# Performance work log

Measured on AMD Instinct MI355X. Metric: run time of the kernel, lower is better.

## Reference

```python
import jax, jax.numpy as jnp
import numpy as np

N, E, F, H, G = 50000, 640000, 128, 128, 64


def setup_inputs() -> dict:
    key = jax.random.key(0)
    ks = jax.random.split(key, 10)
    x = jax.random.normal(ks[0], (N, F), dtype=jnp.float32)
    edge_index = jax.random.randint(ks[1], (2, E), 0, N)
    batch = jnp.sort(jax.random.randint(ks[2], (N,), 0, G))

    def glorot(k, shp):
        return jax.random.normal(k, shp, dtype=jnp.float32) * np.float32(1.0 / np.sqrt(shp[0]))

    W1 = glorot(ks[3], (F, H)); b1 = jnp.zeros((H,), jnp.float32)
    W2 = glorot(ks[4], (H, H)); b2 = jnp.zeros((H,), jnp.float32)
    W3 = glorot(ks[5], (H, H)); b3 = jnp.zeros((H,), jnp.float32)
    W4 = glorot(ks[6], (H, 2)); b4 = jnp.zeros((2,), jnp.float32)
    return {"x": x, "W1": W1, "b1": b1, "W2": W2, "b2": b2,
            "W3": W3, "b3": b3, "W4": W4, "b4": b4,
            "edge_index": edge_index, "batch": batch, "num_graphs": G}


def reference(x, W1, b1, W2, b2, W3, b3, W4, b4, edge_index, batch, num_graphs):
    n = x.shape[0]
    loop = jnp.arange(n, dtype=edge_index.dtype)
    src = jnp.concatenate([edge_index[0], loop])  # with self-loops (PyG GCNConv default)
    dst = jnp.concatenate([edge_index[1], loop])
    # symmetric degree normalization: D^{-1/2} (A+I) D^{-1/2}
    deg = jax.ops.segment_sum(jnp.ones_like(src, dtype=x.dtype), dst, num_segments=n)
    dinv = jnp.where(deg > 0, jax.lax.rsqrt(deg), 0.0)
    norm = (dinv[src] * dinv[dst])[:, None]  # [E+N, 1]

    def gcn_conv(h, W, b):
        m = h @ W                                   # transform first (F->H), then propagate
        agg = jax.ops.segment_sum(m[src] * norm, dst, num_segments=n)
        return agg + b

    h = jax.nn.relu(gcn_conv(x, W1, b1))
    h = jax.nn.relu(gcn_conv(h, W2, b2))
    g = jax.ops.segment_max(h, batch, num_segments=num_graphs)  # global_max_pool
    z = jax.nn.relu(g @ W3 + b3)                    # dropout is identity in eval
    logits = z @ W4 + b4
    return jax.nn.log_softmax(logits, axis=1)
```

## Files before the change

kernel.cpp:

```cpp
#include <hip/hip_runtime.h>
#include <hip/hip_bf16.h>
#include <math.h>

#define HDIM 128
#define SCAN_B 256
#define NBLK 256

typedef short bfrag __attribute__((ext_vector_type(8)));
typedef float f32x4 __attribute__((ext_vector_type(4)));

__device__ inline unsigned short f2bf_rne(float x) {
    unsigned u = __float_as_uint(x);
    u = (u + 0x7fffu + ((u >> 16) & 1u)) >> 16;
    return (unsigned short)u;
}
__device__ inline float bf_lo(unsigned u) { return __uint_as_float(u << 16); }
__device__ inline float bf_hi(unsigned u) { return __uint_as_float(u & 0xffff0000u); }
__device__ inline unsigned bf_pack(float lo, float hi) {
    return ((unsigned)f2bf_rne(hi) << 16) | (unsigned)f2bf_rne(lo);
}


__device__ inline void hist_body(int b, const int* __restrict__ dst,
                                 int* __restrict__ hist, int E, int chunk, int nbuck) {
    __shared__ int hl[256];
    int t = threadIdx.x;
    hl[t] = 0;
    __syncthreads();
    int start = b * chunk, end = min(E, start + chunk);
    for (int e = start + t; e < end; e += 256) atomicAdd(&hl[dst[e] >> 8], 1);
    __syncthreads();
    if (t < nbuck) hist[t * NBLK + b] = hl[t];
}

__device__ inline void wfrag_body(int b, const float* __restrict__ W1,
                                  const float* __restrict__ W2,
                                  unsigned short* __restrict__ w1h,
                                  unsigned short* __restrict__ w1l,
                                  unsigned short* __restrict__ w2h,
                                  unsigned short* __restrict__ w2l) {
    const float* W = (b < 64) ? W1 : W2;
    unsigned short* whi = (b < 64) ? w1h : w2h;
    unsigned short* wlo = (b < 64) ? w1l : w2l;
    int idx = (b & 63) * 256 + threadIdx.x;
    int k = idx >> 7;
    int n = idx & 127;
    int kt = k >> 5, q = (k >> 3) & 3, j = k & 7;
    int lm = n >> 3, nt = n & 7;
    int lane = q * 16 + lm;
    int o = ((kt * 8 + nt) * 64 + lane) * 8 + j;
    float x = W[idx];
    unsigned short hb = f2bf_rne(x);
    float hf = __uint_as_float(((unsigned)hb) << 16);
    unsigned short lb = f2bf_rne(x - hf);
    whi[o] = hb;
    wlo[o] = lb;
}

__device__ inline void scatter_body(int b, const int* __restrict__ srcv,
                                    const int* __restrict__ dstv,
                                    const int* __restrict__ hscan,
                                    int2* __restrict__ sorted,
                                    int E, int chunk, int nbuck) {
    __shared__ int cur[256];
    int t = threadIdx.x;
    if (t < nbuck) cur[t] = hscan[t * NBLK + b];
    __syncthreads();
    int start = b * chunk, end = min(E, start + chunk);
    for (int e = start + t; e < end; e += 256) {
        int d = dstv[e];
        int pos = atomicAdd(&cur[d >> 8], 1);
        sorted[pos] = make_int2(srcv[e], d);
    }
}

#define GBM 64
__device__ inline void gemm_f32_body(int b, const float* __restrict__ A,
                                     const unsigned short* __restrict__ whi,
                                     const unsigned short* __restrict__ wlo,
                                     unsigned short* __restrict__ C, int Nrows) {
    int tid = threadIdx.x;
    int w = tid >> 6, L = tid & 63;
    int lm = L & 15, lq = L >> 4;
    int row0 = b * GBM + w * 16;

    f32x4 acc[8];
#pragma unroll
    for (int nt = 0; nt < 8; ++nt) acc[nt] = (f32x4)(0.f);

#pragma unroll
    for (int kt = 0; kt < 4; ++kt) {
        int gr = row0 + lm;
        float4 v0 = make_float4(0.f, 0.f, 0.f, 0.f);
        float4 v1 = v0;
        if (gr < Nrows) {
            const float* p = &A[(size_t)gr * HDIM + kt * 32 + lq * 8];
            v0 = *(const float4*)p;
            v1 = *(const float4*)(p + 4);
        }
        float xv[8] = {v0.x, v0.y, v0.z, v0.w, v1.x, v1.y, v1.z, v1.w};
        bfrag ah, al;
#pragma unroll
        for (int j = 0; j < 8; ++j) {
            float x = xv[j];
            unsigned short hb = f2bf_rne(x);
            float hf = __uint_as_float(((unsigned)hb) << 16);
            unsigned short lb = f2bf_rne(x - hf);
            ah[j] = (short)hb;
            al[j] = (short)lb;
        }
#pragma unroll
        for (int nt = 0; nt < 8; ++nt) {
            int o = ((kt * 8 + nt) * 64 + L) * 8;
            bfrag wh = *(const bfrag*)&whi[o];
            bfrag wl = *(const bfrag*)&wlo[o];
            acc[nt] = __builtin_amdgcn_mfma_f32_16x16x32_bf16(ah, wh, acc[nt], 0, 0, 0);
            acc[nt] = __builtin_amdgcn_mfma_f32_16x16x32_bf16(al, wh, acc[nt], 0, 0, 0);
            acc[nt] = __builtin_amdgcn_mfma_f32_16x16x32_bf16(ah, wl, acc[nt], 0, 0, 0);
        }
    }

#pragma unroll
    for (int i = 0; i < 4; ++i) {
        int gr = row0 + lq * 4 + i;
        if (gr < Nrows) {
            bfrag e;
#pragma unroll
            for (int nt = 0; nt < 8; ++nt) e[nt] = (short)f2bf_rne(acc[nt][i]);
            *(bfrag*)&C[(size_t)gr * HDIM + lm * 8] = e;
        }
    }
}

__global__ __launch_bounds__(256) void mega1_kernel(const int* __restrict__ dst,
                                                    int* __restrict__ hist, int E,
                                                    int chunk, int nbuck,
                                                    const float* __restrict__ W1,
                                                    const float* __restrict__ W2,
                                                    unsigned short* __restrict__ w1h,
                                                    unsigned short* __restrict__ w1l,
                                                    unsigned short* __restrict__ w2h,
                                                    unsigned short* __restrict__ w2l) {
    int b = blockIdx.x;
    if (b < NBLK) hist_body(b, dst, hist, E, chunk, nbuck);
    else wfrag_body(b - NBLK, W1, W2, w1h, w1l, w2h, w2l);
}

__global__ __launch_bounds__(256) void mega3_kernel(const int* __restrict__ srcv,
                                                    const int* __restrict__ dstv,
                                                    const int* __restrict__ hscan,
                                                    int2* __restrict__ sorted,
                                                    int E, int chunk, int nbuck,
                                                    const float* __restrict__ A,
                                                    const unsigned short* __restrict__ whi,
                                                    const unsigned short* __restrict__ wlo,
                                                    unsigned short* __restrict__ C, int Nrows) {
    int b = blockIdx.x;
    if (b < NBLK) scatter_body(b, srcv, dstv, hscan, sorted, E, chunk, nbuck);
    else gemm_f32_body(b - NBLK, A, whi, wlo, C, Nrows);
}

__global__ __launch_bounds__(SCAN_B) void scan1_kernel(const int* __restrict__ in,
                                                       int* __restrict__ out,
                                                       int* __restrict__ sums, int n) {
    __shared__ int s[SCAN_B];
    int t = threadIdx.x;
    int idx = blockIdx.x * SCAN_B + t;
    int v = (idx < n) ? in[idx] : 0;
    s[t] = v;
    __syncthreads();
    for (int off = 1; off < SCAN_B; off <<= 1) {
        int x = (t >= off) ? s[t - off] : 0;
        __syncthreads();
        s[t] += x;
        __syncthreads();
    }
    if (idx < n) out[idx] = s[t];
    if (t == SCAN_B - 1) sums[blockIdx.x] = s[t];
}

__global__ __launch_bounds__(SCAN_B) void scan2_kernel(int* __restrict__ sums, int nb) {
    __shared__ int s[SCAN_B];
    int t = threadIdx.x;
    int v = (t < nb) ? sums[t] : 0;
    s[t] = v;
    __syncthreads();
    for (int off = 1; off < SCAN_B; off <<= 1) {
        int x = (t >= off) ? s[t - off] : 0;
        __syncthreads();
        s[t] += x;
        __syncthreads();
    }
    if (t < nb) sums[t] = s[t] - v;
}

__global__ __launch_bounds__(SCAN_B) void scan3_kernel(const int* __restrict__ in,
                                                       int* __restrict__ out,
                                                       const int* __restrict__ sums, int n) {
    int idx = blockIdx.x * SCAN_B + threadIdx.x;
    if (idx < n) out[idx] = out[idx] - in[idx] + sums[blockIdx.x];
}

__global__ __launch_bounds__(256) void csr_kernel(const int2* __restrict__ sorted,
                                                  const int* __restrict__ hscan,
                                                  int* __restrict__ rowstart,
                                                  float* __restrict__ dinv,
                                                  int* __restrict__ csr,
                                                  int N, int E, int nbuck) {
    __shared__ int cnt[256];
    __shared__ int s[256];
    __shared__ int cur[256];
    int b = blockIdx.x;
    int t = threadIdx.x;
    int start = hscan[b * NBLK];
    int end = (b + 1 < nbuck) ? hscan[(b + 1) * NBLK] : E;
    cnt[t] = 0;
    __syncthreads();
    for (int e = start + t; e < end; e += 256)
        atomicAdd(&cnt[sorted[e].y & 255], 1);
    __syncthreads();
    int v = cnt[t];
    s[t] = v;
    __syncthreads();
    for (int off = 1; off < 256; off <<= 1) {
        int x = (t >= off) ? s[t - off] : 0;
        __syncthreads();
        s[t] += x;
        __syncthreads();
    }
    int excl = s[t] - v;
    int node = b * 256 + t;
    if (node < N) {
        rowstart[node] = start + excl;
        dinv[node] = rsqrtf((float)(v + 1));
    }
    if (b == nbuck - 1 && t == 0) rowstart[N] = E;
    cur[t] = start + excl;
    __syncthreads();
    for (int e = start + t; e < end; e += 256) {
        int2 ed = sorted[e];
        int pos = atomicAdd(&cur[ed.y & 255], 1);
        csr[pos] = ed.x;
    }
}

#define QACC(UV, WT)                                   \
    acc[0] = fmaf(WT, bf_lo((UV).x), acc[0]);          \
    acc[1] = fmaf(WT, bf_hi((UV).x), acc[1]);          \
    acc[2] = fmaf(WT, bf_lo((UV).y), acc[2]);          \
    acc[3] = fmaf(WT, bf_hi((UV).y), acc[3]);          \
    acc[4] = fmaf(WT, bf_lo((UV).z), acc[4]);          \
    acc[5] = fmaf(WT, bf_hi((UV).z), acc[5]);          \
    acc[6] = fmaf(WT, bf_lo((UV).w), acc[6]);          \
    acc[7] = fmaf(WT, bf_hi((UV).w), acc[7]);

__device__ inline void qgather(const uint4* __restrict__ m4,
                               const int* __restrict__ csr,
                               const float* __restrict__ dinv,
                               int p, int pend, int t, float* acc) {
    for (; p + 8 <= pend; p += 8) {
        int s0 = csr[p], s1 = csr[p + 1], s2 = csr[p + 2], s3 = csr[p + 3];
        int s4 = csr[p + 4], s5 = csr[p + 5], s6 = csr[p + 6], s7 = csr[p + 7];
        float w0 = dinv[s0], w1 = dinv[s1], w2 = dinv[s2], w3 = dinv[s3];
        float w4 = dinv[s4], w5 = dinv[s5], w6 = dinv[s6], w7 = dinv[s7];
        uint4 u0 = m4[(size_t)s0 * 16 + t];
        uint4 u1 = m4[(size_t)s1 * 16 + t];
        uint4 u2 = m4[(size_t)s2 * 16 + t];
        uint4 u3 = m4[(size_t)s3 * 16 + t];
        uint4 u4 = m4[(size_t)s4 * 16 + t];
        uint4 u5 = m4[(size_t)s5 * 16 + t];
        uint4 u6 = m4[(size_t)s6 * 16 + t];
        uint4 u7 = m4[(size_t)s7 * 16 + t];
        QACC(u0, w0); QACC(u1, w1); QACC(u2, w2); QACC(u3, w3);
        QACC(u4, w4); QACC(u5, w5); QACC(u6, w6); QACC(u7, w7);
    }
    if (p + 4 <= pend) {
        int s0 = csr[p], s1 = csr[p + 1], s2 = csr[p + 2], s3 = csr[p + 3];
        float w0 = dinv[s0], w1 = dinv[s1], w2 = dinv[s2], w3 = dinv[s3];
        uint4 u0 = m4[(size_t)s0 * 16 + t];
        uint4 u1 = m4[(size_t)s1 * 16 + t];
        uint4 u2 = m4[(size_t)s2 * 16 + t];
        uint4 u3 = m4[(size_t)s3 * 16 + t];
        QACC(u0, w0); QACC(u1, w1); QACC(u2, w2); QACC(u3, w3);
        p += 4;
    }
    if (p + 2 <= pend) {
        int s0 = csr[p], s1 = csr[p + 1];
        float w0 = dinv[s0], w1 = dinv[s1];
        uint4 u0 = m4[(size_t)s0 * 16 + t];
        uint4 u1 = m4[(size_t)s1 * 16 + t];
        QACC(u0, w0); QACC(u1, w1);
        p += 2;
    }
    if (p < pend) {
        int s0 = csr[p];
        float w0 = dinv[s0];
        uint4 u0 = m4[(size_t)s0 * 16 + t];
        QACC(u0, w0);
    }
}

__global__ __launch_bounds__(256) void agg_gemm_kernel(
        const uint4* __restrict__ m4,
        const int* __restrict__ rowstart,
        const int* __restrict__ csr,
        const float* __restrict__ dinv,
        const float* __restrict__ bias,
        const unsigned short* __restrict__ whi,
        const unsigned short* __restrict__ wlo,
        uint4* __restrict__ out_m, int n) {
    __shared__ unsigned short hbuf[16][HDIM + 8];
    __shared__ float cbuf[16][HDIM + 4];
    int t = threadIdx.x & 15;
    int nl = threadIdx.x >> 4;
    int node = blockIdx.x * 16 + nl;

    unsigned short hv[8] = {0, 0, 0, 0, 0, 0, 0, 0};
    if (node < n) {
        float dd = dinv[node];
        float acc[8];
        uint4 u = m4[(size_t)node * 16 + t];
        acc[0] = dd * bf_lo(u.x); acc[1] = dd * bf_hi(u.x);
        acc[2] = dd * bf_lo(u.y); acc[3] = dd * bf_hi(u.y);
        acc[4] = dd * bf_lo(u.z); acc[5] = dd * bf_hi(u.z);
        acc[6] = dd * bf_lo(u.w); acc[7] = dd * bf_hi(u.w);
        qgather(m4, csr, dinv, rowstart[node], rowstart[node + 1], t, acc);
        float4 b0 = *(const float4*)&bias[t * 8];
        float4 b1 = *(const float4*)&bias[t * 8 + 4];
        float bb[8] = {b0.x, b0.y, b0.z, b0.w, b1.x, b1.y, b1.z, b1.w};
#pragma unroll
        for (int j = 0; j < 8; ++j)
            hv[j] = f2bf_rne(fmaxf(fmaf(dd, acc[j], bb[j]), 0.f));
    }
    *(uint4*)&hbuf[nl][t * 8] = *(uint4*)hv;
    __syncthreads();

    int w = threadIdx.x >> 6, L = threadIdx.x & 63;
    int lm = L & 15, lq = L >> 4;
    f32x4 acc2[2];
    acc2[0] = (f32x4)(0.f);
    acc2[1] = (f32x4)(0.f);
#pragma unroll
    for (int kt = 0; kt < 4; ++kt) {
        bfrag a = *(const bfrag*)&hbuf[lm][kt * 32 + lq * 8];
#pragma unroll
        for (int q2 = 0; q2 < 2; ++q2) {
            int nt = w * 2 + q2;
            int o = ((kt * 8 + nt) * 64 + L) * 8;
            bfrag wh = *(const bfrag*)&whi[o];
            bfrag wl = *(const bfrag*)&wlo[o];
            acc2[q2] = __builtin_amdgcn_mfma_f32_16x16x32_bf16(a, wh, acc2[q2], 0, 0, 0);
            acc2[q2] = __builtin_amdgcn_mfma_f32_16x16x32_bf16(a, wl, acc2[q2], 0, 0, 0);
        }
    }
#pragma unroll
    for (int q2 = 0; q2 < 2; ++q2) {
        int nt = w * 2 + q2;
#pragma unroll
        for (int i = 0; i < 4; ++i) cbuf[lq * 4 + i][lm * 8 + nt] = acc2[q2][i];
    }
    __syncthreads();

    if (node < n) {
        float4 r0 = *(const float4*)&cbuf[nl][t * 8];
        float4 r1 = *(const float4*)&cbuf[nl][t * 8 + 4];
        unsigned short ev[8];
        ev[0] = f2bf_rne(r0.x); ev[1] = f2bf_rne(r0.y);
        ev[2] = f2bf_rne(r0.z); ev[3] = f2bf_rne(r0.w);
        ev[4] = f2bf_rne(r1.x); ev[5] = f2bf_rne(r1.y);
        ev[6] = f2bf_rne(r1.z); ev[7] = f2bf_rne(r1.w);
        out_m[(size_t)node * 16 + t] = *(uint4*)ev;
    }
}

__global__ __launch_bounds__(256) void agg_pool_kernel(const uint4* __restrict__ m4,
                                                       const int* __restrict__ rowstart,
                                                       const int* __restrict__ csr,
                                                       const float* __restrict__ dinv,
                                                       const float* __restrict__ bias,
                                                       const int* __restrict__ batch,
                                                       unsigned int* __restrict__ g, int n) {
    __shared__ float smx[16][HDIM];
    __shared__ int sgid[16];
    int t = threadIdx.x & 15;
    int nl = threadIdx.x >> 4;
    int node = blockIdx.x * 16 + nl;
    bool valid = node < n;
    if (valid) {
        float dd = dinv[node];
        float acc[8];
        uint4 u = m4[(size_t)node * 16 + t];
        acc[0] = dd * bf_lo(u.x); acc[1] = dd * bf_hi(u.x);
        acc[2] = dd * bf_lo(u.y); acc[3] = dd * bf_hi(u.y);
        acc[4] = dd * bf_lo(u.z); acc[5] = dd * bf_hi(u.z);
        acc[6] = dd * bf_lo(u.w); acc[7] = dd * bf_hi(u.w);
        qgather(m4, csr, dinv, rowstart[node], rowstart[node + 1], t, acc);
        float4 b0 = *(const float4*)&bias[t * 8];
        float4 b1 = *(const float4*)&bias[t * 8 + 4];
        float4 r0, r1;
        r0.x = fmaxf(fmaf(dd, acc[0], b0.x), 0.f);
        r0.y = fmaxf(fmaf(dd, acc[1], b0.y), 0.f);
        r0.z = fmaxf(fmaf(dd, acc[2], b0.z), 0.f);
        r0.w = fmaxf(fmaf(dd, acc[3], b0.w), 0.f);
        r1.x = fmaxf(fmaf(dd, acc[4], b1.x), 0.f);
        r1.y = fmaxf(fmaf(dd, acc[5], b1.y), 0.f);
        r1.z = fmaxf(fmaf(dd, acc[6], b1.z), 0.f);
        r1.w = fmaxf(fmaf(dd, acc[7], b1.w), 0.f);
        *(float4*)&smx[nl][t * 8] = r0;
        *(float4*)&smx[nl][t * 8 + 4] = r1;
    }
    if (t == 0) sgid[nl] = valid ? batch[node] : -1;
    __syncthreads();
    if (threadIdx.x < HDIM) {
        int c = threadIdx.x;
        int curg = -1;
        float run = 0.f;
#pragma unroll
        for (int r = 0; r < 16; ++r) {
            int gg = sgid[r];
            if (gg < 0) continue;
            if (gg != curg) {
                if (curg >= 0) atomicMax(&g[curg * HDIM + c], __float_as_uint(run));
                curg = gg;
                run = smx[r][c];
            } else {
                run = fmaxf(run, smx[r][c]);
            }
        }
        if (curg >= 0) atomicMax(&g[curg * HDIM + c], __float_as_uint(run));
    }
}

__global__ __launch_bounds__(128) void mlp_kernel(const unsigned int* __restrict__ gbits,
                                                  const float* __restrict__ W3,
                                                  const float* __restrict__ b3,
                                                  const float* __restrict__ W4,
                                                  const float* __restrict__ b4,
                                                  float* __restrict__ out) {
    __shared__ float gs[HDIM];
    __shared__ float r0[HDIM];
    __shared__ float r1[HDIM];
    int j = threadIdx.x;
    int b = blockIdx.x;
    gs[j] = __uint_as_float(gbits[b * HDIM + j]);
    __syncthreads();
    float acc = b3[j];
#pragma unroll 8
    for (int k = 0; k < HDIM; ++k) acc = fmaf(gs[k], W3[k * HDIM + j], acc);
    float z = fmaxf(acc, 0.f);
    r0[j] = z * W4[j * 2 + 0];
    r1[j] = z * W4[j * 2 + 1];
    __syncthreads();
    for (int off = 64; off > 0; off >>= 1) {
        if (j < off) {
            r0[j] += r0[j + off];
            r1[j] += r1[j + off];
        }
        __syncthreads();
    }
    if (j == 0) {
        float l0 = r0[0] + b4[0];
        float l1 = r1[0] + b4[1];
        float mx = fmaxf(l0, l1);
        float lse = mx + logf(expf(l0 - mx) + expf(l1 - mx));
        out[b * 2 + 0] = l0 - lse;
        out[b * 2 + 1] = l1 - lse;
    }
}

extern "C" void kernel_launch(void* const* d_in, const int* in_sizes, int n_in,
                              void* d_out, int out_size, void* d_ws, size_t ws_size,
                              hipStream_t stream) {
    const float* x  = (const float*)d_in[0];
    const float* W1 = (const float*)d_in[1];
    const float* b1 = (const float*)d_in[2];
    const float* W2 = (const float*)d_in[3];
    const float* b2 = (const float*)d_in[4];
    const float* W3 = (const float*)d_in[5];
    const float* b3 = (const float*)d_in[6];
    const float* W4 = (const float*)d_in[7];
    const float* b4 = (const float*)d_in[8];
    const int* ei    = (const int*)d_in[9];
    const int* batch = (const int*)d_in[10];

    const int N = in_sizes[0] / HDIM;
    const int E = in_sizes[9] / 2;
    const int G = out_size / 2;
    const int* src = ei;
    const int* dst = ei + E;

    const int nbuck = (N + 255) >> 8;
    const int nscan = nbuck * NBLK;
    const int chunk = (E + NBLK - 1) / NBLK;

    const int Nr = ((N + 63) / 64) * 64;
    char* wsb = (char*)d_ws;
    size_t o = 0;
    unsigned int* g = (unsigned int*)(wsb + o); o += (size_t)G * HDIM * 4;
    size_t zero_bytes = o;
    int* hist = (int*)(wsb + o);           o += (size_t)nscan * 4;
    int* hscan = (int*)(wsb + o);          o += (size_t)nscan * 4;
    int* sums = (int*)(wsb + o);           o += 256 * 4;
    int* rowstart = (int*)(wsb + o);       o += (size_t)(Nr + 64) * 4;
    float* dinv = (float*)(wsb + o);       o += (size_t)Nr * 4;
    int2* sorted = (int2*)(wsb + o);       o += (size_t)E * 8;
    int* csr = (int*)(wsb + o);            o += (size_t)E * 4;
    unsigned short* wf1h = (unsigned short*)(wsb + o); o += (size_t)HDIM * HDIM * 2;
    unsigned short* wf1l = (unsigned short*)(wsb + o); o += (size_t)HDIM * HDIM * 2;
    unsigned short* wf2h = (unsigned short*)(wsb + o); o += (size_t)HDIM * HDIM * 2;
    unsigned short* wf2l = (unsigned short*)(wsb + o); o += (size_t)HDIM * HDIM * 2;
    unsigned short* m = (unsigned short*)(wsb + o);    o += (size_t)Nr * HDIM * 2;
    unsigned short* m2 = (unsigned short*)(wsb + o);   o += (size_t)Nr * HDIM * 2;
    (void)ws_size; (void)n_in;

    (void)hipMemsetAsync(d_ws, 0, zero_bytes, stream);

    int sblocks = (nscan + SCAN_B - 1) / SCAN_B;
    int gemm_blocks = (N + GBM - 1) / GBM;
    int agg_blocks = (N + 15) / 16;

    mega1_kernel<<<NBLK + 128, 256, 0, stream>>>(dst, hist, E, chunk, nbuck,
                                                 W1, W2, wf1h, wf1l, wf2h, wf2l);
    scan1_kernel<<<sblocks, SCAN_B, 0, stream>>>(hist, hscan, sums, nscan);
    scan2_kernel<<<1, SCAN_B, 0, stream>>>(sums, sblocks);
    scan3_kernel<<<sblocks, SCAN_B, 0, stream>>>(hist, hscan, sums, nscan);
    mega3_kernel<<<NBLK + gemm_blocks, 256, 0, stream>>>(src, dst, hscan, sorted,
                                                         E, chunk, nbuck,
                                                         x, wf1h, wf1l, m, N);
    csr_kernel<<<nbuck, 256, 0, stream>>>(sorted, hscan, rowstart, dinv, csr, N, E, nbuck);
    agg_gemm_kernel<<<agg_blocks, 256, 0, stream>>>((const uint4*)m, rowstart, csr,
                                                    dinv, b1, wf2h, wf2l,
                                                    (uint4*)m2, N);
    agg_pool_kernel<<<agg_blocks, 256, 0, stream>>>((const uint4*)m2, rowstart, csr,
                                                    dinv, b2, batch, g, N);
    mlp_kernel<<<G, 128, 0, stream>>>(g, W3, b3, W4, b4, (float*)d_out);
}
```

Before: 201.7 us.

## Pack sorted edges into int, merge scan passes, process two nodes per aggregation thread

Sorted edge records shrink from an int2 to a single int, with the source id in the low 16 bits and the low byte of the destination above it. This halves the scatter and CSR-build traffic, but source ids only fit while N < 65536. The separate sum-scan kernel is folded into the final scan pass, so every block redundantly rescans the block sums in exchange for one fewer launch. The aggregation kernels now handle 32 nodes per block, and each thread gathers two nodes' neighbor lists in an interleaved loop for more memory-level parallelism, at the cost of more registers and fewer blocks.

```diff
diff --git a/kernel.cpp b/kernel.cpp
--- a/kernel.cpp
+++ b/kernel.cpp
@@ -16,9 +16,6 @@
 }
 __device__ inline float bf_lo(unsigned u) { return __uint_as_float(u << 16); }
 __device__ inline float bf_hi(unsigned u) { return __uint_as_float(u & 0xffff0000u); }
-__device__ inline unsigned bf_pack(float lo, float hi) {
-    return ((unsigned)f2bf_rne(hi) << 16) | (unsigned)f2bf_rne(lo);
-}
 
 
 __device__ inline void hist_body(int b, const int* __restrict__ dst,
@@ -60,7 +57,7 @@
 __device__ inline void scatter_body(int b, const int* __restrict__ srcv,
                                     const int* __restrict__ dstv,
                                     const int* __restrict__ hscan,
-                                    int2* __restrict__ sorted,
+                                    int* __restrict__ sorted,
                                     int E, int chunk, int nbuck) {
     __shared__ int cur[256];
     int t = threadIdx.x;
@@ -70,7 +67,7 @@
     for (int e = start + t; e < end; e += 256) {
         int d = dstv[e];
         int pos = atomicAdd(&cur[d >> 8], 1);
-        sorted[pos] = make_int2(srcv[e], d);
+        sorted[pos] = srcv[e] | ((d & 255) << 16);
     }
 }
 
@@ -149,7 +146,7 @@
 __global__ __launch_bounds__(256) void mega3_kernel(const int* __restrict__ srcv,
                                                     const int* __restrict__ dstv,
                                                     const int* __restrict__ hscan,
-                                                    int2* __restrict__ sorted,
+                                                    int* __restrict__ sorted,
                                                     int E, int chunk, int nbuck,
                                                     const float* __restrict__ A,
                                                     const unsigned short* __restrict__ whi,
@@ -179,7 +176,10 @@
     if (t == SCAN_B - 1) sums[blockIdx.x] = s[t];
 }
 
-__global__ __launch_bounds__(SCAN_B) void scan2_kernel(int* __restrict__ sums, int nb) {
+__global__ __launch_bounds__(SCAN_B) void scan3_kernel(const int* __restrict__ in,
+                                                       int* __restrict__ out,
+                                                       const int* __restrict__ sums,
+                                                       int n, int nb) {
     __shared__ int s[SCAN_B];
     int t = threadIdx.x;
     int v = (t < nb) ? sums[t] : 0;
@@ -191,17 +191,12 @@
         s[t] += x;
         __syncthreads();
     }
-    if (t < nb) sums[t] = s[t] - v;
-}
-
-__global__ __launch_bounds__(SCAN_B) void scan3_kernel(const int* __restrict__ in,
-                                                       int* __restrict__ out,
-                                                       const int* __restrict__ sums, int n) {
-    int idx = blockIdx.x * SCAN_B + threadIdx.x;
-    if (idx < n) out[idx] = out[idx] - in[idx] + sums[blockIdx.x];
-}
-
-__global__ __launch_bounds__(256) void csr_kernel(const int2* __restrict__ sorted,
+    int base = (blockIdx.x > 0) ? s[blockIdx.x - 1] : 0;
+    int idx = blockIdx.x * SCAN_B + t;
+    if (idx < n) out[idx] = out[idx] - in[idx] + base;
+}
+
+__global__ __launch_bounds__(256) void csr_kernel(const int* __restrict__ sorted,
                                                   const int* __restrict__ hscan,
                                                   int* __restrict__ rowstart,
                                                   float* __restrict__ dinv,
@@ -217,7 +212,7 @@
     cnt[t] = 0;
     __syncthreads();
     for (int e = start + t; e < end; e += 256)
-        atomicAdd(&cnt[sorted[e].y & 255], 1);
+        atomicAdd(&cnt[(sorted[e] >> 16) & 255], 1);
     __syncthreads();
     int v = cnt[t];
     s[t] = v;
@@ -238,21 +233,21 @@
     cur[t] = start + excl;
     __syncthreads();
     for (int e = start + t; e < end; e += 256) {
-        int2 ed = sorted[e];
-        int pos = atomicAdd(&cur[ed.y & 255], 1);
-        csr[pos] = ed.x;
-    }
-}
-
-#define QACC(UV, WT)                                   \
-    acc[0] = fmaf(WT, bf_lo((UV).x), acc[0]);          \
-    acc[1] = fmaf(WT, bf_hi((UV).x), acc[1]);          \
-    acc[2] = fmaf(WT, bf_lo((UV).y), acc[2]);          \
-    acc[3] = fmaf(WT, bf_hi((UV).y), acc[3]);          \
-    acc[4] = fmaf(WT, bf_lo((UV).z), acc[4]);          \
-    acc[5] = fmaf(WT, bf_hi((UV).z), acc[5]);          \
-    acc[6] = fmaf(WT, bf_lo((UV).w), acc[6]);          \
-    acc[7] = fmaf(WT, bf_hi((UV).w), acc[7]);
+        int ed = sorted[e];
+        int pos = atomicAdd(&cur[(ed >> 16) & 255], 1);
+        csr[pos] = ed & 0xFFFF;
+    }
+}
+
+#define QACC(ACCP, UV, WT)                                 \
+    ACCP[0] = fmaf(WT, bf_lo((UV).x), ACCP[0]);            \
+    ACCP[1] = fmaf(WT, bf_hi((UV).x), ACCP[1]);            \
+    ACCP[2] = fmaf(WT, bf_lo((UV).y), ACCP[2]);            \
+    ACCP[3] = fmaf(WT, bf_hi((UV).y), ACCP[3]);            \
+    ACCP[4] = fmaf(WT, bf_lo((UV).z), ACCP[4]);            \
+    ACCP[5] = fmaf(WT, bf_hi((UV).z), ACCP[5]);            \
+    ACCP[6] = fmaf(WT, bf_lo((UV).w), ACCP[6]);            \
+    ACCP[7] = fmaf(WT, bf_hi((UV).w), ACCP[7]);
 
 __device__ inline void qgather(const uint4* __restrict__ m4,
                                const int* __restrict__ csr,
@@ -271,8 +266,8 @@
         uint4 u5 = m4[(size_t)s5 * 16 + t];
         uint4 u6 = m4[(size_t)s6 * 16 + t];
         uint4 u7 = m4[(size_t)s7 * 16 + t];
-        QACC(u0, w0); QACC(u1, w1); QACC(u2, w2); QACC(u3, w3);
-        QACC(u4, w4); QACC(u5, w5); QACC(u6, w6); QACC(u7, w7);
+        QACC(acc, u0, w0); QACC(acc, u1, w1); QACC(acc, u2, w2); QACC(acc, u3, w3);
+        QACC(acc, u4, w4); QACC(acc, u5, w5); QACC(acc, u6, w6); QACC(acc, u7, w7);
     }
     if (p + 4 <= pend) {
         int s0 = csr[p], s1 = csr[p + 1], s2 = csr[p + 2], s3 = csr[p + 3];
@@ -281,7 +276,7 @@
         uint4 u1 = m4[(size_t)s1 * 16 + t];
         uint4 u2 = m4[(size_t)s2 * 16 + t];
         uint4 u3 = m4[(size_t)s3 * 16 + t];
-        QACC(u0, w0); QACC(u1, w1); QACC(u2, w2); QACC(u3, w3);
+        QACC(acc, u0, w0); QACC(acc, u1, w1); QACC(acc, u2, w2); QACC(acc, u3, w3);
         p += 4;
     }
     if (p + 2 <= pend) {
@@ -289,15 +284,41 @@
         float w0 = dinv[s0], w1 = dinv[s1];
         uint4 u0 = m4[(size_t)s0 * 16 + t];
         uint4 u1 = m4[(size_t)s1 * 16 + t];
-        QACC(u0, w0); QACC(u1, w1);
+        QACC(acc, u0, w0); QACC(acc, u1, w1);
         p += 2;
     }
     if (p < pend) {
         int s0 = csr[p];
         float w0 = dinv[s0];
         uint4 u0 = m4[(size_t)s0 * 16 + t];
-        QACC(u0, w0);
-    }
+        QACC(acc, u0, w0);
+    }
+}
+
+__device__ inline void qgather2(const uint4* __restrict__ m4,
+                                const int* __restrict__ csr,
+                                const float* __restrict__ dinv,
+                                int pA, int eA, int pB, int eB, int t,
+                                float* accA, float* accB) {
+    while (pA + 4 <= eA && pB + 4 <= eB) {
+        int a0 = csr[pA], a1 = csr[pA + 1], a2 = csr[pA + 2], a3 = csr[pA + 3];
+        int b0 = csr[pB], b1 = csr[pB + 1], b2 = csr[pB + 2], b3 = csr[pB + 3];
+        float va0 = dinv[a0], va1 = dinv[a1], va2 = dinv[a2], va3 = dinv[a3];
+        float vb0 = dinv[b0], vb1 = dinv[b1], vb2 = dinv[b2], vb3 = dinv[b3];
+        uint4 ua0 = m4[(size_t)a0 * 16 + t];
+        uint4 ua1 = m4[(size_t)a1 * 16 + t];
+        uint4 ua2 = m4[(size_t)a2 * 16 + t];
+        uint4 ua3 = m4[(size_t)a3 * 16 + t];
+        uint4 ub0 = m4[(size_t)b0 * 16 + t];
+        uint4 ub1 = m4[(size_t)b1 * 16 + t];
+        uint4 ub2 = m4[(size_t)b2 * 16 + t];
+        uint4 ub3 = m4[(size_t)b3 * 16 + t];
+        QACC(accA, ua0, va0); QACC(accA, ua1, va1); QACC(accA, ua2, va2); QACC(accA, ua3, va3);
+        QACC(accB, ub0, vb0); QACC(accB, ub1, vb1); QACC(accB, ub2, vb2); QACC(accB, ub3, vb3);
+        pA += 4; pB += 4;
+    }
+    qgather(m4, csr, dinv, pA, eA, t, accA);
+    qgather(m4, csr, dinv, pB, eB, t, accB);
 }
 
 __global__ __launch_bounds__(256) void agg_gemm_kernel(
@@ -309,59 +330,89 @@
         const unsigned short* __restrict__ whi,
         const unsigned short* __restrict__ wlo,
         uint4* __restrict__ out_m, int n) {
-    __shared__ unsigned short hbuf[16][HDIM + 8];
-    __shared__ float cbuf[16][HDIM + 4];
+    __shared__ unsigned short hbuf[32][HDIM + 8];
+    __shared__ float cbuf[32][HDIM + 4];
     int t = threadIdx.x & 15;
     int nl = threadIdx.x >> 4;
-    int node = blockIdx.x * 16 + nl;
-
-    unsigned short hv[8] = {0, 0, 0, 0, 0, 0, 0, 0};
-    if (node < n) {
-        float dd = dinv[node];
-        float acc[8];
-        uint4 u = m4[(size_t)node * 16 + t];
-        acc[0] = dd * bf_lo(u.x); acc[1] = dd * bf_hi(u.x);
-        acc[2] = dd * bf_lo(u.y); acc[3] = dd * bf_hi(u.y);
-        acc[4] = dd * bf_lo(u.z); acc[5] = dd * bf_hi(u.z);
-        acc[6] = dd * bf_lo(u.w); acc[7] = dd * bf_hi(u.w);
-        qgather(m4, csr, dinv, rowstart[node], rowstart[node + 1], t, acc);
-        float4 b0 = *(const float4*)&bias[t * 8];
-        float4 b1 = *(const float4*)&bias[t * 8 + 4];
-        float bb[8] = {b0.x, b0.y, b0.z, b0.w, b1.x, b1.y, b1.z, b1.w};
-#pragma unroll
-        for (int j = 0; j < 8; ++j)
-            hv[j] = f2bf_rne(fmaxf(fmaf(dd, acc[j], bb[j]), 0.f));
-    }
-    *(uint4*)&hbuf[nl][t * 8] = *(uint4*)hv;
+    int nodeA = blockIdx.x * 32 + nl;
+    int nodeB = nodeA + 16;
+    bool vA = nodeA < n, vB = nodeB < n;
+
+    float accA[8], accB[8];
+    float ddA = 0.f, ddB = 0.f;
+    int pA = 0, eA = 0, pB = 0, eB = 0;
+    if (vA) {
+        ddA = dinv[nodeA];
+        uint4 u = m4[(size_t)nodeA * 16 + t];
+        accA[0] = ddA * bf_lo(u.x); accA[1] = ddA * bf_hi(u.x);
+        accA[2] = ddA * bf_lo(u.y); accA[3] = ddA * bf_hi(u.y);
+        accA[4] = ddA * bf_lo(u.z); accA[5] = ddA * bf_hi(u.z);
+        accA[6] = ddA * bf_lo(u.w); accA[7] = ddA * bf_hi(u.w);
+        pA = rowstart[nodeA]; eA = rowstart[nodeA + 1];
+    } else {
+#pragma unroll
+        for (int j = 0; j < 8; ++j) accA[j] = 0.f;
+    }
+    if (vB) {
+        ddB = dinv[nodeB];
+        uint4 u = m4[(size_t)nodeB * 16 + t];
+        accB[0] = ddB * bf_lo(u.x); accB[1] = ddB * bf_hi(u.x);
+        accB[2] = ddB * bf_lo(u.y); accB[3] = ddB * bf_hi(u.y);
+        accB[4] = ddB * bf_lo(u.z); accB[5] = ddB * bf_hi(u.z);
+        accB[6] = ddB * bf_lo(u.w); accB[7] = ddB * bf_hi(u.w);
+        pB = rowstart[nodeB]; eB = rowstart[nodeB + 1];
+    } else {
+#pragma unroll
+        for (int j = 0; j < 8; ++j) accB[j] = 0.f;
+    }
+    qgather2(m4, csr, dinv, pA, eA, pB, eB, t, accA, accB);
+
+    float4 b0 = *(const float4*)&bias[t * 8];
+    float4 b1 = *(const float4*)&bias[t * 8 + 4];
+    float bb[8] = {b0.x, b0.y, b0.z, b0.w, b1.x, b1.y, b1.z, b1.w};
+    unsigned short hA[8], hB[8];
+#pragma unroll
+    for (int j = 0; j < 8; ++j) {
+        hA[j] = vA ? f2bf_rne(fmaxf(fmaf(ddA, accA[j], bb[j]), 0.f)) : (unsigned short)0;
+        hB[j] = vB ? f2bf_rne(fmaxf(fmaf(ddB, accB[j], bb[j]), 0.f)) : (unsigned short)0;
+    }
+    *(uint4*)&hbuf[nl][t * 8] = *(uint4*)hA;
+    *(uint4*)&hbuf[nl + 16][t * 8] = *(uint4*)hB;
     __syncthreads();
 
     int w = threadIdx.x >> 6, L = threadIdx.x & 63;
     int lm = L & 15, lq = L >> 4;
-    f32x4 acc2[2];
-    acc2[0] = (f32x4)(0.f);
-    acc2[1] = (f32x4)(0.f);
+    f32x4 acc2[2][2];
+    acc2[0][0] = (f32x4)(0.f); acc2[0][1] = (f32x4)(0.f);
+    acc2[1][0] = (f32x4)(0.f); acc2[1][1] = (f32x4)(0.f);
 #pragma unroll
     for (int kt = 0; kt < 4; ++kt) {
-        bfrag a = *(const bfrag*)&hbuf[lm][kt * 32 + lq * 8];
+        bfrag a0r = *(const bfrag*)&hbuf[lm][kt * 32 + lq * 8];
+        bfrag a1r = *(const bfrag*)&hbuf[16 + lm][kt * 32 + lq * 8];
 #pragma unroll
         for (int q2 = 0; q2 < 2; ++q2) {
             int nt = w * 2 + q2;
             int o = ((kt * 8 + nt) * 64 + L) * 8;
             bfrag wh = *(const bfrag*)&whi[o];
             bfrag wl = *(const bfrag*)&wlo[o];
-            acc2[q2] = __builtin_amdgcn_mfma_f32_16x16x32_bf16(a, wh, acc2[q2], 0, 0, 0);
-            acc2[q2] = __builtin_amdgcn_mfma_f32_16x16x32_bf16(a, wl, acc2[q2], 0, 0, 0);
-        }
-    }
-#pragma unroll
-    for (int q2 = 0; q2 < 2; ++q2) {
-        int nt = w * 2 + q2;
-#pragma unroll
-        for (int i = 0; i < 4; ++i) cbuf[lq * 4 + i][lm * 8 + nt] = acc2[q2][i];
-    }
-    __syncthreads();
-
-    if (node < n) {
+            acc2[0][q2] = __builtin_amdgcn_mfma_f32_16x16x32_bf16(a0r, wh, acc2[0][q2], 0, 0, 0);
+            acc2[0][q2] = __builtin_amdgcn_mfma_f32_16x16x32_bf16(a0r, wl, acc2[0][q2], 0, 0, 0);
+            acc2[1][q2] = __builtin_amdgcn_mfma_f32_16x16x32_bf16(a1r, wh, acc2[1][q2], 0, 0, 0);
+            acc2[1][q2] = __builtin_amdgcn_mfma_f32_16x16x32_bf16(a1r, wl, acc2[1][q2], 0, 0, 0);
+        }
+    }
+#pragma unroll
+    for (int mt = 0; mt < 2; ++mt)
+#pragma unroll
+        for (int q2 = 0; q2 < 2; ++q2) {
+            int nt = w * 2 + q2;
+#pragma unroll
+            for (int i = 0; i < 4; ++i)
+                cbuf[mt * 16 + lq * 4 + i][lm * 8 + nt] = acc2[mt][q2][i];
+        }
+    __syncthreads();
+
+    if (vA) {
         float4 r0 = *(const float4*)&cbuf[nl][t * 8];
         float4 r1 = *(const float4*)&cbuf[nl][t * 8 + 4];
         unsigned short ev[8];
@@ -369,7 +420,17 @@
         ev[2] = f2bf_rne(r0.z); ev[3] = f2bf_rne(r0.w);
         ev[4] = f2bf_rne(r1.x); ev[5] = f2bf_rne(r1.y);
         ev[6] = f2bf_rne(r1.z); ev[7] = f2bf_rne(r1.w);
-        out_m[(size_t)node * 16 + t] = *(uint4*)ev;
+        out_m[(size_t)nodeA * 16 + t] = *(uint4*)ev;
+    }
+    if (vB) {
+        float4 r0 = *(const float4*)&cbuf[nl + 16][t * 8];
+        float4 r1 = *(const float4*)&cbuf[nl + 16][t * 8 + 4];
+        unsigned short ev[8];
+        ev[0] = f2bf_rne(r0.x); ev[1] = f2bf_rne(r0.y);
+        ev[2] = f2bf_rne(r0.z); ev[3] = f2bf_rne(r0.w);
+        ev[4] = f2bf_rne(r1.x); ev[5] = f2bf_rne(r1.y);
+        ev[6] = f2bf_rne(r1.z); ev[7] = f2bf_rne(r1.w);
+        out_m[(size_t)nodeB * 16 + t] = *(uint4*)ev;
     }
 }
 
@@ -380,43 +441,62 @@
                                                        const float* __restrict__ bias,
                                                        const int* __restrict__ batch,
                                                        unsigned int* __restrict__ g, int n) {
-    __shared__ float smx[16][HDIM];
-    __shared__ int sgid[16];
+    __shared__ float smx[32][HDIM];
+    __shared__ int sgid[32];
     int t = threadIdx.x & 15;
     int nl = threadIdx.x >> 4;
-    int node = blockIdx.x * 16 + nl;
-    bool valid = node < n;
-    if (valid) {
-        float dd = dinv[node];
-        float acc[8];
-        uint4 u = m4[(size_t)node * 16 + t];
-        acc[0] = dd * bf_lo(u.x); acc[1] = dd * bf_hi(u.x);
-        acc[2] = dd * bf_lo(u.y); acc[3] = dd * bf_hi(u.y);
-        acc[4] = dd * bf_lo(u.z); acc[5] = dd * bf_hi(u.z);
-        acc[6] = dd * bf_lo(u.w); acc[7] = dd * bf_hi(u.w);
-        qgather(m4, csr, dinv, rowstart[node], rowstart[node + 1], t, acc);
-        float4 b0 = *(const float4*)&bias[t * 8];
-        float4 b1 = *(const float4*)&bias[t * 8 + 4];
-        float4 r0, r1;
-        r0.x = fmaxf(fmaf(dd, acc[0], b0.x), 0.f);
-        r0.y = fmaxf(fmaf(dd, acc[1], b0.y), 0.f);
-        r0.z = fmaxf(fmaf(dd, acc[2], b0.z), 0.f);
-        r0.w = fmaxf(fmaf(dd, acc[3], b0.w), 0.f);
-        r1.x = fmaxf(fmaf(dd, acc[4], b1.x), 0.f);
-        r1.y = fmaxf(fmaf(dd, acc[5], b1.y), 0.f);
-        r1.z = fmaxf(fmaf(dd, acc[6], b1.z), 0.f);
-        r1.w = fmaxf(fmaf(dd, acc[7], b1.w), 0.f);
-        *(float4*)&smx[nl][t * 8] = r0;
-        *(float4*)&smx[nl][t * 8 + 4] = r1;
-    }
-    if (t == 0) sgid[nl] = valid ? batch[node] : -1;
+    int nodeA = blockIdx.x * 32 + nl;
+    int nodeB = nodeA + 16;
+    bool vA = nodeA < n, vB = nodeB < n;
+
+    float accA[8], accB[8];
+    float ddA = 0.f, ddB = 0.f;
+    int pA = 0, eA = 0, pB = 0, eB = 0;
+    if (vA) {
+        ddA = dinv[nodeA];
+        uint4 u = m4[(size_t)nodeA * 16 + t];
+        accA[0] = ddA * bf_lo(u.x); accA[1] = ddA * bf_hi(u.x);
+        accA[2] = ddA * bf_lo(u.y); accA[3] = ddA * bf_hi(u.y);
+        accA[4] = ddA * bf_lo(u.z); accA[5] = ddA * bf_hi(u.z);
+        accA[6] = ddA * bf_lo(u.w); accA[7] = ddA * bf_hi(u.w);
+        pA = rowstart[nodeA]; eA = rowstart[nodeA + 1];
+    } else {
+#pragma unroll
+        for (int j = 0; j < 8; ++j) accA[j] = 0.f;
+    }
+    if (vB) {
+        ddB = dinv[nodeB];
+        uint4 u = m4[(size_t)nodeB * 16 + t];
+        accB[0] = ddB * bf_lo(u.x); accB[1] = ddB * bf_hi(u.x);
+        accB[2] = ddB * bf_lo(u.y); accB[3] = ddB * bf_hi(u.y);
+        accB[4] = ddB * bf_lo(u.z); accB[5] = ddB * bf_hi(u.z);
+        accB[6] = ddB * bf_lo(u.w); accB[7] = ddB * bf_hi(u.w);
+        pB = rowstart[nodeB]; eB = rowstart[nodeB + 1];
+    } else {
+#pragma unroll
+        for (int j = 0; j < 8; ++j) accB[j] = 0.f;
+    }
+    qgather2(m4, csr, dinv, pA, eA, pB, eB, t, accA, accB);
+
+    float4 b0 = *(const float4*)&bias[t * 8];
+    float4 b1 = *(const float4*)&bias[t * 8 + 4];
+    float bb[8] = {b0.x, b0.y, b0.z, b0.w, b1.x, b1.y, b1.z, b1.w};
+#pragma unroll
+    for (int j = 0; j < 8; ++j) {
+        smx[nl][t * 8 + j] = vA ? fmaxf(fmaf(ddA, accA[j], bb[j]), 0.f) : 0.f;
+        smx[nl + 16][t * 8 + j] = vB ? fmaxf(fmaf(ddB, accB[j], bb[j]), 0.f) : 0.f;
+    }
+    if (t == 0) {
+        sgid[nl] = vA ? batch[nodeA] : -1;
+        sgid[nl + 16] = vB ? batch[nodeB] : -1;
+    }
     __syncthreads();
     if (threadIdx.x < HDIM) {
         int c = threadIdx.x;
         int curg = -1;
         float run = 0.f;
 #pragma unroll
-        for (int r = 0; r < 16; ++r) {
+        for (int r = 0; r < 32; ++r) {
             int gg = sgid[r];
             if (gg < 0) continue;
             if (gg != curg) {
@@ -503,7 +583,7 @@
     int* sums = (int*)(wsb + o);           o += 256 * 4;
     int* rowstart = (int*)(wsb + o);       o += (size_t)(Nr + 64) * 4;
     float* dinv = (float*)(wsb + o);       o += (size_t)Nr * 4;
-    int2* sorted = (int2*)(wsb + o);       o += (size_t)E * 8;
+    int* sorted = (int*)(wsb + o);         o += (size_t)E * 4;
     int* csr = (int*)(wsb + o);            o += (size_t)E * 4;
     unsigned short* wf1h = (unsigned short*)(wsb + o); o += (size_t)HDIM * HDIM * 2;
     unsigned short* wf1l = (unsigned short*)(wsb + o); o += (size_t)HDIM * HDIM * 2;
@@ -517,13 +597,12 @@
 
     int sblocks = (nscan + SCAN_B - 1) / SCAN_B;
     int gemm_blocks = (N + GBM - 1) / GBM;
-    int agg_blocks = (N + 15) / 16;
+    int agg_blocks = (N + 31) / 32;
 
     mega1_kernel<<<NBLK + 128, 256, 0, stream>>>(dst, hist, E, chunk, nbuck,
                                                  W1, W2, wf1h, wf1l, wf2h, wf2l);
     scan1_kernel<<<sblocks, SCAN_B, 0, stream>>>(hist, hscan, sums, nscan);
-    scan2_kernel<<<1, SCAN_B, 0, stream>>>(sums, sblocks);
-    scan3_kernel<<<sblocks, SCAN_B, 0, stream>>>(hist, hscan, sums, nscan);
+    scan3_kernel<<<sblocks, SCAN_B, 0, stream>>>(hist, hscan, sums, nscan, sblocks);
     mega3_kernel<<<NBLK + gemm_blocks, 256, 0, stream>>>(src, dst, hscan, sorted,
                                                          E, chunk, nbuck,
                                                          x, wf1h, wf1l, m, N);
```

New measurement: 212.8 us. 1.06x slower.
